# Performance work log

Measured on AMD Instinct MI355X. Metric: run time of the kernel, lower is better.

Reference implementation:

```python
import jax, jax.numpy as jnp
import numpy as np

B, T, D_MODEL, H, D = 2, 2048, 2048, 16, 128


def _rope_tables(t, d_half, base=10000.0):
    inv_freq = 1.0 / (base ** (jnp.arange(d_half, dtype=jnp.float32) / d_half))
    ang = jnp.arange(t, dtype=jnp.float32)[:, None] * inv_freq[None, :]  # (T, D/2)
    return jnp.cos(ang), jnp.sin(ang)


def setup_inputs() -> dict:
    key = jax.random.key(0)
    ks = jax.random.split(key, 5)
    x = jax.random.normal(ks[0], (B, T, D_MODEL), dtype=jnp.float32)
    mask = jnp.tril(jnp.ones((T, T), dtype=bool))  # causal boolean mask
    cos, sin = _rope_tables(T, D // 2)
    std = 1.0 / np.sqrt(D_MODEL)
    Wq = jax.random.normal(ks[1], (D_MODEL, H * D), dtype=jnp.float32) * std
    Wk = jax.random.normal(ks[2], (D_MODEL, H * D), dtype=jnp.float32) * std
    Wv = jax.random.normal(ks[3], (D_MODEL, H * D), dtype=jnp.float32) * std
    Wo = jax.random.normal(ks[4], (H * D, D_MODEL), dtype=jnp.float32) * std
    return {"x": x, "mask": mask, "cos": cos, "sin": sin,
            "Wq": Wq, "Wk": Wk, "Wv": Wv, "Wo": Wo}


def _apply_rope(x, cos, sin):
    # x: (B, H, T, D); cos/sin: (T, D/2)
    half = x.shape[-1] // 2
    x1, x2 = x[..., :half], x[..., half:]
    c = cos[None, None]
    s = sin[None, None]
    return jnp.concatenate([x1 * c - x2 * s, x1 * s + x2 * c], axis=-1)


def reference(x, mask, cos, sin, Wq, Wk, Wv, Wo):
    b, t, _ = x.shape
    scale = 1.0 / np.sqrt(D)
    # projections: (B, T, H*D) -> (B, H, T, D)
    q = (x @ Wq).reshape(b, t, H, D).transpose(0, 2, 1, 3)
    k = (x @ Wk).reshape(b, t, H, D).transpose(0, 2, 1, 3)
    v = (x @ Wv).reshape(b, t, H, D).transpose(0, 2, 1, 3)
    q = _apply_rope(q, cos, sin)
    k = _apply_rope(k, cos, sin)
    scores = jnp.einsum('bhqd,bhkd->bhqk', q, k) * scale
    scores = jnp.where(mask[None, None], scores, jnp.float32(-1e30))
    attn = jax.nn.softmax(scores, axis=-1)
    out = jnp.einsum('bhqk,bhkd->bhqd', attn, v)  # (B, H, T, D)
    out = out.transpose(0, 2, 1, 3).reshape(b, t, H * D)
    return out @ Wo
```

## Files before the change

kernel.cpp:

```cpp
#include <hip/hip_runtime.h>

#define T_SEQ 2048
#define DM    2048
#define NH    16
#define HD    128
#define NROW  4096

typedef __attribute__((ext_vector_type(8))) short short8;
typedef __attribute__((ext_vector_type(4))) float f32x4;
typedef __attribute__((ext_vector_type(16))) float f32x16;

static __device__ __forceinline__ float bf2f(unsigned short h) {
    unsigned int u = ((unsigned int)h) << 16;
    return __builtin_bit_cast(float, u);
}
static __device__ __forceinline__ unsigned short f2bf(float f) {
    unsigned int u = __builtin_bit_cast(unsigned int, f);
    u += 0x7FFFu + ((u >> 16) & 1u);
    return (unsigned short)(u >> 16);
}
static __device__ __forceinline__ unsigned short bf_fast(float f) {
    return (unsigned short)((__builtin_bit_cast(unsigned int, f) + 0x8000u) >> 16);
}

typedef __attribute__((address_space(1))) const unsigned int gas_uint;
typedef __attribute__((address_space(3))) unsigned int las_uint;

static __device__ __forceinline__ void load_lds16(const void* g, void* l) {
    __builtin_amdgcn_global_load_lds((gas_uint*)g, (las_uint*)l, 16, 0, 0);
}

static __device__ __forceinline__ f32x4 mfma_bf16(short8 a, short8 b, f32x4 c) {
    return __builtin_amdgcn_mfma_f32_16x16x32_bf16(a, b, c, 0, 0, 0);
}
static __device__ __forceinline__ f32x16 mfma32_bf16(short8 a, short8 b, f32x16 c) {
    return __builtin_amdgcn_mfma_f32_32x32x16_bf16(a, b, c, 0, 0, 0);
}

__global__ __launch_bounds__(256) void k_prep(const float* __restrict__ x,
                                              unsigned short* __restrict__ xb,
                                              const float* __restrict__ w0, const float* __restrict__ w1,
                                              const float* __restrict__ w2, const float* __restrict__ w3,
                                              unsigned short* __restrict__ t0, unsigned short* __restrict__ t1,
                                              unsigned short* __restrict__ t2, unsigned short* __restrict__ t3) {
    const int tid = threadIdx.x;
    const int z = blockIdx.z;
    if (z == 4) {
        const int iblock = blockIdx.y * 32 + blockIdx.x;
#pragma unroll
        for (int i = 0; i < 8; ++i) {
            int idx = (iblock * 2048 + i * 256 + tid) * 4;
            float4 v = *(const float4*)(x + idx);
            ushort4 o;
            o.x = f2bf(v.x); o.y = f2bf(v.y); o.z = f2bf(v.z); o.w = f2bf(v.w);
            *(ushort4*)(xb + idx) = o;
        }
        return;
    }
    __shared__ unsigned short tile[64][68];
    const float* W = (z == 0) ? w0 : (z == 1) ? w1 : (z == 2) ? w2 : w3;
    unsigned short* Wt = (z == 0) ? t0 : (z == 1) ? t1 : (z == 2) ? t2 : t3;
    const int bx = blockIdx.x * 64;
    const int by = blockIdx.y * 64;
    const int rr = tid >> 4, cc = (tid & 15) * 4;
#pragma unroll
    for (int it = 0; it < 4; ++it) {
        int row = it * 16 + rr;
        float4 v = *(const float4*)(W + (size_t)(by + row) * DM + bx + cc);
        ushort4 o;
        o.x = f2bf(v.x); o.y = f2bf(v.y); o.z = f2bf(v.z); o.w = f2bf(v.w);
        *(ushort4*)&tile[row][cc] = o;
    }
    __syncthreads();
#pragma unroll
    for (int it = 0; it < 4; ++it) {
        int ln = it * 16 + rr;
        ushort4 v;
#pragma unroll
        for (int j = 0; j < 4; ++j) v = (j == 0) ? (ushort4){tile[cc][ln], 0, 0, 0} : v, ((unsigned short*)&v)[j] = tile[cc + j][ln];
        *(ushort4*)(Wt + (size_t)(bx + ln) * DM + by + cc) = v;
    }
}

template <bool FOUT>
static __device__ __forceinline__ void gemm_body(const unsigned short* __restrict__ A,
                                                 const unsigned short* __restrict__ Bt,
                                                 unsigned short* __restrict__ Cb,
                                                 float* __restrict__ Cf) {
    __shared__ unsigned short As[128 * 64];
    __shared__ unsigned short Bs[128 * 64];
    const int tid = threadIdx.x;
    const int w = tid >> 6, lane = tid & 63;
    const int col = lane & 15, quad = lane >> 4;
    const int wm = w >> 1, wn = w & 1;
    const size_t m0 = (size_t)blockIdx.y * 128;
    const size_t n0 = (size_t)blockIdx.x * 128;

    f32x4 acc[4][4];
#pragma unroll
    for (int i = 0; i < 4; ++i)
#pragma unroll
        for (int j = 0; j < 4; ++j)
            acc[i][j] = (f32x4){0.f, 0.f, 0.f, 0.f};

    const int lrow = lane >> 3;
    const int gcol = ((lane & 7) ^ lrow) * 8;

    for (int k0 = 0; k0 < DM; k0 += 64) {
#pragma unroll
        for (int c = w; c < 16; c += 4) {
            load_lds16(A + (m0 + c * 8 + lrow) * DM + k0 + gcol, &As[c * 512]);
            load_lds16(Bt + (n0 + c * 8 + lrow) * DM + k0 + gcol, &Bs[c * 512]);
        }
        __syncthreads();
#pragma unroll
        for (int ks = 0; ks < 2; ++ks) {
            short8 af[4], bf[4];
            int g = ks * 4 + quad;
#pragma unroll
            for (int mt = 0; mt < 4; ++mt) {
                int r = wm * 64 + mt * 16 + col;
                af[mt] = *(const short8*)&As[r * 64 + ((g ^ (r & 7)) * 8)];
            }
#pragma unroll
            for (int nt = 0; nt < 4; ++nt) {
                int r = wn * 64 + nt * 16 + col;
                bf[nt] = *(const short8*)&Bs[r * 64 + ((g ^ (r & 7)) * 8)];
            }
#pragma unroll
            for (int mt = 0; mt < 4; ++mt)
#pragma unroll
                for (int nt = 0; nt < 4; ++nt)
                    acc[mt][nt] = mfma_bf16(af[mt], bf[nt], acc[mt][nt]);
        }
        __syncthreads();
    }
#pragma unroll
    for (int mt = 0; mt < 4; ++mt)
#pragma unroll
        for (int nt = 0; nt < 4; ++nt)
#pragma unroll
            for (int reg = 0; reg < 4; ++reg) {
                size_t r = m0 + wm * 64 + mt * 16 + quad * 4 + reg;
                size_t c = n0 + wn * 64 + nt * 16 + col;
                if (FOUT) Cf[r * DM + c] = acc[mt][nt][reg];
                else      Cb[r * DM + c] = f2bf(acc[mt][nt][reg]);
            }
}

__global__ __launch_bounds__(256) void k_gemm_qkv(const unsigned short* __restrict__ xb,
                                                  const unsigned short* __restrict__ wtq,
                                                  const unsigned short* __restrict__ wtk,
                                                  const unsigned short* __restrict__ wtv,
                                                  unsigned short* __restrict__ qb,
                                                  unsigned short* __restrict__ kb,
                                                  unsigned short* __restrict__ vb) {
    int z = blockIdx.z;
    const unsigned short* Bt = (z == 0) ? wtq : (z == 1) ? wtk : wtv;
    unsigned short* C = (z == 0) ? qb : (z == 1) ? kb : vb;
    gemm_body<false>(xb, Bt, C, nullptr);
}

__global__ __launch_bounds__(256) void k_gemm_out(const unsigned short* __restrict__ ob,
                                                  const unsigned short* __restrict__ wto,
                                                  float* __restrict__ out) {
    gemm_body<true>(ob, wto, nullptr, out);
}

__global__ __launch_bounds__(256) void k_rope_k(unsigned short* __restrict__ K,
                                                const float* __restrict__ cosp,
                                                const float* __restrict__ sinp) {
    int idx = blockIdx.x * 256 + threadIdx.x;
    int d4 = (idx & 15) * 4;
    int h = (idx >> 4) & 15;
    int row = idx >> 8;
    int t = row & (T_SEQ - 1);
    size_t base = (size_t)row * DM + h * HD + d4;
    ushort4 x1 = *(const ushort4*)(K + base);
    ushort4 x2 = *(const ushort4*)(K + base + 64);
    float4 c = *(const float4*)(cosp + t * 64 + d4);
    float4 s = *(const float4*)(sinp + t * 64 + d4);
    ushort4 o1, o2;
#pragma unroll
    for (int i = 0; i < 4; ++i) {
        float a1 = bf2f(((const unsigned short*)&x1)[i]);
        float a2 = bf2f(((const unsigned short*)&x2)[i]);
        float cc = ((const float*)&c)[i], ss = ((const float*)&s)[i];
        ((unsigned short*)&o1)[i] = f2bf(a1 * cc - a2 * ss);
        ((unsigned short*)&o2)[i] = f2bf(a1 * ss + a2 * cc);
    }
    *(ushort4*)(K + base) = o1;
    *(ushort4*)(K + base + 64) = o2;
}

__global__ __launch_bounds__(256) void k_vtr(const unsigned short* __restrict__ V,
                                             unsigned short* __restrict__ Vt) {
    __shared__ unsigned short tile[64][68];
    int t0 = blockIdx.x * 64;
    int hd0 = blockIdx.y * 64;
    int b = blockIdx.z;
    int tid = threadIdx.x;
    int rr = tid >> 4, cc = (tid & 15) * 4;
#pragma unroll
    for (int it = 0; it < 4; ++it) {
        int row = it * 16 + rr;
        *(ushort4*)&tile[row][cc] =
            *(const ushort4*)(V + (size_t)(b * T_SEQ + t0 + row) * DM + hd0 + cc);
    }
    __syncthreads();
    int h = hd0 >> 7, d0 = hd0 & 127;
    size_t obase = (size_t)(b * NH + h) * HD;
#pragma unroll
    for (int it = 0; it < 4; ++it) {
        int lhd = it * 16 + rr;
        ushort4 v;
#pragma unroll
        for (int j = 0; j < 4; ++j) ((unsigned short*)&v)[j] = tile[cc + j][lhd];
        *(ushort4*)(Vt + (obase + d0 + lhd) * (size_t)T_SEQ + t0 + cc) = v;
    }
}

#define PST 72
__global__ __launch_bounds__(256) void k_flash(const unsigned short* __restrict__ Q,
                                               const unsigned short* __restrict__ K,
                                               const unsigned short* __restrict__ Vt,
                                               unsigned short* __restrict__ O,
                                               const float* __restrict__ cosp,
                                               const float* __restrict__ sinp) {
    __shared__ unsigned short Ks[64 * 128];
    __shared__ unsigned short Vs[128 * 64];
    __shared__ unsigned short Ps[4][32 * PST];
    const int tid = threadIdx.x;
    const int w = tid >> 6, lane = tid & 63;
    const int col = lane & 31, l5 = lane >> 5;
    const int flat = blockIdx.x | (blockIdx.y << 4) | (blockIdx.z << 8);
    const int j = 15 - (flat >> 5);
    const int hb = flat & 31;
    const int h = hb & 15, b = hb >> 4;
    const int q0 = j * 128;
    const size_t rowbase = ((size_t)b * T_SEQ) * DM + (size_t)h * HD;
    const size_t hbase = ((size_t)b * NH + h) * HD;
    const float SCL = 0.088388347648318447f * 1.4426950408889634f;
    unsigned short* Pw = &Ps[w][0];

    const int t = q0 + w * 32 + col;
    short8 qf[8];
    {
        const unsigned short* qp = Q + rowbase + (size_t)t * DM + l5 * 8;
#pragma unroll
        for (int st = 0; st < 8; ++st)
            qf[st] = *(const short8*)(qp + st * 16);
        const float* cp = cosp + t * 64 + l5 * 8;
        const float* sp = sinp + t * 64 + l5 * 8;
#pragma unroll
        for (int st = 0; st < 4; ++st) {
            float4 c0 = *(const float4*)(cp + st * 16);
            float4 c1 = *(const float4*)(cp + st * 16 + 4);
            float4 s0v = *(const float4*)(sp + st * 16);
            float4 s1v = *(const float4*)(sp + st * 16 + 4);
#pragma unroll
            for (int jj = 0; jj < 8; ++jj) {
                float cv = ((jj < 4) ? ((const float*)&c0)[jj] : ((const float*)&c1)[jj - 4]) * SCL;
                float sv = ((jj < 4) ? ((const float*)&s0v)[jj] : ((const float*)&s1v)[jj - 4]) * SCL;
                float a1 = bf2f((unsigned short)qf[st][jj]);
                float a2 = bf2f((unsigned short)qf[st + 4][jj]);
                qf[st][jj]     = (short)f2bf(a1 * cv - a2 * sv);
                qf[st + 4][jj] = (short)f2bf(a1 * sv + a2 * cv);
            }
        }
    }

    f32x16 o[4];
#pragma unroll
    for (int i = 0; i < 4; ++i) o[i] = (f32x16)(0.f);
    float m_i = -1e30f, l_i = 0.f;

    const int kt_max = 2 * j + 1;
    const int kt_lim = (q0 + w * 32 + 31) >> 6;
    const int cswz = col & 7;

    for (int kt = 0; kt <= kt_max; ++kt) {
        const int k0 = kt * 64;
        __syncthreads();
#pragma unroll
        for (int c = 0; c < 4; ++c) {
            const int c4 = w * 4 + c;
            const int krow = c4 * 4 + (lane >> 4);
            const int kpos = lane & 15;
            load_lds16(K + rowbase + (size_t)(k0 + krow) * DM + ((kpos ^ (krow & 7)) * 8),
                       &Ks[c4 * 512]);
            const int vrow = c4 * 8 + (lane >> 3);
            const int vpos = lane & 7;
            load_lds16(Vt + (hbase + vrow) * (size_t)T_SEQ + k0 + ((vpos ^ (vrow & 7)) * 8),
                       &Vs[c4 * 512]);
        }
        __syncthreads();
        if (kt > kt_lim) continue;

        f32x16 s0 = (f32x16)(0.f), s1 = (f32x16)(0.f);
#pragma unroll
        for (int st = 0; st < 8; ++st) {
            const int dg = (2 * st + l5) ^ cswz;
            short8 kf0 = *(const short8*)&Ks[col * 128 + dg * 8];
            short8 kf1 = *(const short8*)&Ks[col * 128 + 4096 + dg * 8];
            s0 = mfma32_bf16(kf0, qf[st], s0);
            s1 = mfma32_bf16(kf1, qf[st], s1);
        }

        if (k0 + 63 > q0 + w * 32) {
            const int kb = k0 + 4 * l5;
#pragma unroll
            for (int r = 0; r < 16; ++r) {
                const int key = kb + (r & 3) + 8 * (r >> 2);
                if (key > t) s0[r] = -1e30f;
                if (key + 32 > t) s1[r] = -1e30f;
            }
        }

        float mx = -1e30f;
#pragma unroll
        for (int r = 0; r < 16; ++r) mx = fmaxf(mx, fmaxf(s0[r], s1[r]));
        mx = fmaxf(mx, __shfl_xor(mx, 32));
        const float mnew = fmaxf(m_i, mx);
        const float alpha = __builtin_amdgcn_exp2f(m_i - mnew);
        m_i = mnew;
        float sum = 0.f;
#pragma unroll
        for (int r = 0; r < 16; ++r) {
            float p0 = __builtin_amdgcn_exp2f(s0[r] - mnew);
            float p1 = __builtin_amdgcn_exp2f(s1[r] - mnew);
            s0[r] = p0; s1[r] = p1;
            sum += p0 + p1;
        }
        sum += __shfl_xor(sum, 32);
        l_i = l_i * alpha + sum;
#pragma unroll
        for (int i = 0; i < 4; ++i) o[i] *= alpha;

#pragma unroll
        for (int g = 0; g < 4; ++g) {
            ushort4 a4, b4;
#pragma unroll
            for (int i = 0; i < 4; ++i) {
                ((unsigned short*)&a4)[i] = bf_fast(s0[g * 4 + i]);
                ((unsigned short*)&b4)[i] = bf_fast(s1[g * 4 + i]);
            }
            *(ushort4*)(Pw + col * PST + g * 8 + 4 * l5)      = a4;
            *(ushort4*)(Pw + col * PST + 32 + g * 8 + 4 * l5) = b4;
        }
        short8 pb[4];
#pragma unroll
        for (int st = 0; st < 4; ++st)
            pb[st] = *(const short8*)(Pw + col * PST + st * 16 + l5 * 8);

#pragma unroll
        for (int ms = 0; ms < 4; ++ms) {
            const int drow = (ms * 32 + col) * 64;
#pragma unroll
            for (int st = 0; st < 4; ++st) {
                const int kg = (2 * st + l5) ^ cswz;
                short8 vf = *(const short8*)&Vs[drow + kg * 8];
                o[ms] = mfma32_bf16(vf, pb[st], o[ms]);
            }
        }
    }

    const float inv = __builtin_amdgcn_rcpf(l_i);
    unsigned short* op = O + rowbase + (size_t)t * DM;
#pragma unroll
    for (int ms = 0; ms < 4; ++ms)
#pragma unroll
        for (int g = 0; g < 4; ++g) {
            ushort4 st4;
#pragma unroll
            for (int i = 0; i < 4; ++i)
                ((unsigned short*)&st4)[i] = bf_fast(o[ms][g * 4 + i] * inv);
            *(ushort4*)(op + ms * 32 + g * 8 + 4 * l5) = st4;
        }
}

extern "C" void kernel_launch(void* const* d_in, const int* in_sizes, int n_in,
                              void* d_out, int out_size, void* d_ws, size_t ws_size,
                              hipStream_t stream) {
    const float* x    = (const float*)d_in[0];
    const float* cosp = (const float*)d_in[2];
    const float* sinp = (const float*)d_in[3];
    const float* Wq   = (const float*)d_in[4];
    const float* Wk   = (const float*)d_in[5];
    const float* Wv   = (const float*)d_in[6];
    const float* Wo   = (const float*)d_in[7];
    float* out = (float*)d_out;

    unsigned short* xb  = (unsigned short*)d_ws;
    unsigned short* wtq = xb  + (size_t)NROW * DM;
    unsigned short* wtk = wtq + (size_t)DM * DM;
    unsigned short* wtv = wtk + (size_t)DM * DM;
    unsigned short* wto = wtv + (size_t)DM * DM;
    unsigned short* qb  = wto + (size_t)DM * DM;
    unsigned short* kb  = qb  + (size_t)NROW * DM;
    unsigned short* vb  = kb  + (size_t)NROW * DM;
    unsigned short* ob  = vb  + (size_t)NROW * DM;
    unsigned short* vt  = xb;

    hipLaunchKernelGGL(k_prep, dim3(32, 32, 5), dim3(256), 0, stream,
                       x, xb, Wq, Wk, Wv, Wo, wtq, wtk, wtv, wto);
    hipLaunchKernelGGL(k_gemm_qkv, dim3(16, 32, 3), dim3(256), 0, stream,
                       xb, wtq, wtk, wtv, qb, kb, vb);
    hipLaunchKernelGGL(k_rope_k, dim3(4096), dim3(256), 0, stream, kb, cosp, sinp);
    hipLaunchKernelGGL(k_vtr, dim3(32, 32, 2), dim3(256), 0, stream, vb, vt);
    hipLaunchKernelGGL(k_flash, dim3(16, 16, 2), dim3(256), 0, stream,
                       qb, kb, vt, ob, cosp, sinp);
    hipLaunchKernelGGL(k_gemm_out, dim3(16, 32, 1), dim3(256), 0, stream, ob, wto, out);
}
```

Measured before the change: 387.7 us.

## Double-buffer GEMM LDS tiles with 256x128 blocks and XCD-aware block swizzle

Rewrites the shared bf16 GEMM body used by the QKV and output projections. It now uses 512-thread blocks computing 256x128 tiles, with the global-to-LDS loads of the next K tile issued before computing on the current one. A manual vmcnt wait replaces the two __syncthreads per iteration, and s_setprio raises priority around the MFMA section. The launch is a flat grid whose block index is swizzled so neighbouring tiles land on the same XCD, improving L2 reuse. The cost is 96KB of LDS per block, which limits occupancy to one block per CU despite the launch bounds hint.

```diff
diff --git a/kernel.cpp b/kernel.cpp
--- a/kernel.cpp
+++ b/kernel.cpp
@@ -86,15 +86,14 @@
 static __device__ __forceinline__ void gemm_body(const unsigned short* __restrict__ A,
                                                  const unsigned short* __restrict__ Bt,
                                                  unsigned short* __restrict__ Cb,
-                                                 float* __restrict__ Cf) {
-    __shared__ unsigned short As[128 * 64];
-    __shared__ unsigned short Bs[128 * 64];
+                                                 float* __restrict__ Cf,
+                                                 int m0, int n0) {
+    __shared__ unsigned short As[2][256 * 64];
+    __shared__ unsigned short Bs[2][128 * 64];
     const int tid = threadIdx.x;
     const int w = tid >> 6, lane = tid & 63;
     const int col = lane & 15, quad = lane >> 4;
     const int wm = w >> 1, wn = w & 1;
-    const size_t m0 = (size_t)blockIdx.y * 128;
-    const size_t n0 = (size_t)blockIdx.x * 128;
 
     f32x4 acc[4][4];
 #pragma unroll
@@ -104,67 +103,95 @@
             acc[i][j] = (f32x4){0.f, 0.f, 0.f, 0.f};
 
     const int lrow = lane >> 3;
-    const int gcol = ((lane & 7) ^ lrow) * 8;
-
-    for (int k0 = 0; k0 < DM; k0 += 64) {
-#pragma unroll
-        for (int c = w; c < 16; c += 4) {
-            load_lds16(A + (m0 + c * 8 + lrow) * DM + k0 + gcol, &As[c * 512]);
-            load_lds16(Bt + (n0 + c * 8 + lrow) * DM + k0 + gcol, &Bs[c * 512]);
-        }
-        __syncthreads();
+    const int gswz = ((lane & 7) ^ (lrow & 7)) * 8;
+    const unsigned short* Abase = A  + (size_t)(m0 + w * 8 + lrow) * DM + gswz;
+    const unsigned short* Bbase = Bt + (size_t)(n0 + w * 8 + lrow) * DM + gswz;
+
+#define STG_TILE(b_, kk_) do {                                                  \
+    load_lds16(Abase + (size_t)(kk_),                  &As[b_][0 * 4096 + w * 512]); \
+    load_lds16(Abase + 64 * (size_t)DM + (kk_),        &As[b_][1 * 4096 + w * 512]); \
+    load_lds16(Abase + 128 * (size_t)DM + (kk_),       &As[b_][2 * 4096 + w * 512]); \
+    load_lds16(Abase + 192 * (size_t)DM + (kk_),       &As[b_][3 * 4096 + w * 512]); \
+    load_lds16(Bbase + (size_t)(kk_),                  &Bs[b_][0 * 4096 + w * 512]); \
+    load_lds16(Bbase + 64 * (size_t)DM + (kk_),        &Bs[b_][1 * 4096 + w * 512]); \
+} while (0)
+
+    STG_TILE(0, 0);
+
+    const int NT = DM / 64;
+    for (int t = 0; t < NT; ++t) {
+        const int buf = t & 1;
+        if (t + 1 < NT) {
+            STG_TILE(buf ^ 1, (t + 1) * 64);
+            asm volatile("s_waitcnt vmcnt(6)" ::: "memory");
+        } else {
+            asm volatile("s_waitcnt vmcnt(0)" ::: "memory");
+        }
+        __builtin_amdgcn_s_barrier();
+        __builtin_amdgcn_sched_barrier(0);
+
 #pragma unroll
         for (int ks = 0; ks < 2; ++ks) {
-            short8 af[4], bf[4];
-            int g = ks * 4 + quad;
+            short8 af[4], bfr[4];
+            const int g = ks * 4 + quad;
 #pragma unroll
             for (int mt = 0; mt < 4; ++mt) {
-                int r = wm * 64 + mt * 16 + col;
-                af[mt] = *(const short8*)&As[r * 64 + ((g ^ (r & 7)) * 8)];
+                const int r = wm * 64 + mt * 16 + col;
+                af[mt] = *(const short8*)&As[buf][r * 64 + ((g ^ (r & 7)) * 8)];
             }
 #pragma unroll
             for (int nt = 0; nt < 4; ++nt) {
-                int r = wn * 64 + nt * 16 + col;
-                bf[nt] = *(const short8*)&Bs[r * 64 + ((g ^ (r & 7)) * 8)];
-            }
+                const int rb = wn * 64 + nt * 16 + col;
+                bfr[nt] = *(const short8*)&Bs[buf][rb * 64 + ((g ^ (rb & 7)) * 8)];
+            }
+            __builtin_amdgcn_s_setprio(1);
 #pragma unroll
             for (int mt = 0; mt < 4; ++mt)
 #pragma unroll
                 for (int nt = 0; nt < 4; ++nt)
-                    acc[mt][nt] = mfma_bf16(af[mt], bf[nt], acc[mt][nt]);
-        }
-        __syncthreads();
-    }
+                    acc[mt][nt] = mfma_bf16(af[mt], bfr[nt], acc[mt][nt]);
+            __builtin_amdgcn_s_setprio(0);
+        }
+        __builtin_amdgcn_s_barrier();
+    }
+#undef STG_TILE
+
 #pragma unroll
     for (int mt = 0; mt < 4; ++mt)
 #pragma unroll
         for (int nt = 0; nt < 4; ++nt)
 #pragma unroll
             for (int reg = 0; reg < 4; ++reg) {
-                size_t r = m0 + wm * 64 + mt * 16 + quad * 4 + reg;
-                size_t c = n0 + wn * 64 + nt * 16 + col;
+                size_t r = (size_t)m0 + wm * 64 + mt * 16 + quad * 4 + reg;
+                size_t c = (size_t)n0 + wn * 64 + nt * 16 + col;
                 if (FOUT) Cf[r * DM + c] = acc[mt][nt][reg];
                 else      Cb[r * DM + c] = f2bf(acc[mt][nt][reg]);
             }
 }
 
-__global__ __launch_bounds__(256) void k_gemm_qkv(const unsigned short* __restrict__ xb,
-                                                  const unsigned short* __restrict__ wtq,
-                                                  const unsigned short* __restrict__ wtk,
-                                                  const unsigned short* __restrict__ wtv,
-                                                  unsigned short* __restrict__ qb,
-                                                  unsigned short* __restrict__ kb,
-                                                  unsigned short* __restrict__ vb) {
-    int z = blockIdx.z;
-    const unsigned short* Bt = (z == 0) ? wtq : (z == 1) ? wtk : wtv;
-    unsigned short* C = (z == 0) ? qb : (z == 1) ? kb : vb;
-    gemm_body<false>(xb, Bt, C, nullptr);
-}
-
-__global__ __launch_bounds__(256) void k_gemm_out(const unsigned short* __restrict__ ob,
-                                                  const unsigned short* __restrict__ wto,
-                                                  float* __restrict__ out) {
-    gemm_body<true>(ob, wto, nullptr, out);
+__global__ __launch_bounds__(512, 2) void k_gemm_qkv(const unsigned short* __restrict__ xb,
+                                                     const unsigned short* __restrict__ wtq,
+                                                     const unsigned short* __restrict__ wtk,
+                                                     const unsigned short* __restrict__ wtv,
+                                                     unsigned short* __restrict__ qb,
+                                                     unsigned short* __restrict__ kb,
+                                                     unsigned short* __restrict__ vb) {
+    const int flat = blockIdx.x;
+    const int swz = (flat & 7) * 96 + (flat >> 3);
+    const int tz = swz >> 8, rem = swz & 255;
+    const int tx = rem & 15, ty = rem >> 4;
+    const unsigned short* Bt = (tz == 0) ? wtq : (tz == 1) ? wtk : wtv;
+    unsigned short* C = (tz == 0) ? qb : (tz == 1) ? kb : vb;
+    gemm_body<false>(xb, Bt, C, nullptr, ty * 256, tx * 128);
+}
+
+__global__ __launch_bounds__(512, 2) void k_gemm_out(const unsigned short* __restrict__ ob,
+                                                     const unsigned short* __restrict__ wto,
+                                                     float* __restrict__ out) {
+    const int flat = blockIdx.x;
+    const int swz = (flat & 7) * 32 + (flat >> 3);
+    const int tx = swz & 15, ty = swz >> 4;
+    gemm_body<true>(ob, wto, nullptr, out, ty * 256, tx * 128);
 }
 
 __global__ __launch_bounds__(256) void k_rope_k(unsigned short* __restrict__ K,
@@ -404,11 +431,11 @@
 
     hipLaunchKernelGGL(k_prep, dim3(32, 32, 5), dim3(256), 0, stream,
                        x, xb, Wq, Wk, Wv, Wo, wtq, wtk, wtv, wto);
-    hipLaunchKernelGGL(k_gemm_qkv, dim3(16, 32, 3), dim3(256), 0, stream,
+    hipLaunchKernelGGL(k_gemm_qkv, dim3(768), dim3(512), 0, stream,
                        xb, wtq, wtk, wtv, qb, kb, vb);
     hipLaunchKernelGGL(k_rope_k, dim3(4096), dim3(256), 0, stream, kb, cosp, sinp);
     hipLaunchKernelGGL(k_vtr, dim3(32, 32, 2), dim3(256), 0, stream, vb, vt);
     hipLaunchKernelGGL(k_flash, dim3(16, 16, 2), dim3(256), 0, stream,
                        qb, kb, vt, ob, cosp, sinp);
-    hipLaunchKernelGGL(k_gemm_out, dim3(16, 32, 1), dim3(256), 0, stream, ob, wto, out);
-}
+    hipLaunchKernelGGL(k_gemm_out, dim3(256), dim3(512), 0, stream, ob, wto, out);
+}
```

After: 426.2 us. 9.9% more time.
